# Performance work log

Hardware: AMD Instinct MI355X
Metric: run time of the kernel (lower is better)

The kernel has to match this reference:

```python
import jax, jax.numpy as jnp
import numpy as np

B, H, L, DK = 1, 16, 2048, 64
F_FACTOR = 64            # f
MAX_SEQ = 2048           # max_seq_len
RB = MAX_SEQ // F_FACTOR # 32, out dim of f_b


def setup_inputs() -> dict:
    key = jax.random.key(0)
    ks = jax.random.split(key, 6)
    q = jax.random.normal(ks[0], (B, H, L, DK), dtype=jnp.float32)
    v = jax.random.normal(ks[1], (B, H, L, DK), dtype=jnp.float32)
    # nn.Linear weights: [out_features, in_features]
    Wa = jax.random.normal(ks[2], (F_FACTOR, DK), dtype=jnp.float32) / np.sqrt(DK)
    ba = jax.random.normal(ks[3], (F_FACTOR,), dtype=jnp.float32) * 0.02
    Wb = jax.random.normal(ks[4], (RB, DK), dtype=jnp.float32) / np.sqrt(DK)
    bb = jax.random.normal(ks[5], (RB,), dtype=jnp.float32) * 0.02
    return {"q": q, "v": v, "Wa": Wa, "ba": ba, "Wb": Wb, "bb": bb, "len_q": L}


def reference(q, v, Wa, ba, Wb, bb, len_q):
    f = Wa.shape[0]            # f
    rb = Wb.shape[0]           # max_seq_len // f
    # h_a: repeat each of the f factor channels (max_seq_len//f) times -> [B,H,L,max_seq_len], slice to len_q
    h_a = jnp.repeat(q @ Wa.T + ba, rb, axis=-1)[..., :len_q]
    # h_b: repeat each of the (max_seq_len//f) channels f times
    h_b = jnp.repeat(q @ Wb.T + bb, f, axis=-1)[..., :len_q]
    # dense_attn = h_a @ h_b^T  -> [B,H,L,L]
    dense_attn = jnp.einsum('bhik,bhjk->bhij', h_a, h_b)
    # mask=None path; dropout inactive (eval / p=0)
    dense_attn = jax.nn.softmax(dense_attn, axis=-1)
    output = jnp.matmul(dense_attn, v)  # [B,H,L,DK]
    return (output, dense_attn)
```

## Files before the change

kernel.cpp:

```cpp
#include <hip/hip_runtime.h>
#include <hip/hip_bf16.h>


#define HN 16
#define LN 2048
#define KR 32

typedef __attribute__((ext_vector_type(8))) short bf16x8;
typedef __attribute__((ext_vector_type(4))) float f32x4;

__device__ __forceinline__ float b2f(unsigned short u) {
    return __uint_as_float(((unsigned int)u) << 16);
}
__device__ __forceinline__ unsigned short f2b(float f) {
    __hip_bfloat16 h = __float2bfloat16(f);
    return *reinterpret_cast<unsigned short*>(&h);
}
__device__ __forceinline__ void glds16(const void* g, void* l) {
    __builtin_amdgcn_global_load_lds(
        (const __attribute__((address_space(1))) unsigned int*)g,
        (__attribute__((address_space(3))) unsigned int*)l, 16, 0, 0);
}

#define TILE_SH 8192

__global__ __launch_bounds__(256) void k_cb(
    const float* __restrict__ q,
    const float* __restrict__ Wa, const float* __restrict__ ba,
    const float* __restrict__ Wb, const float* __restrict__ bb,
    unsigned short* __restrict__ Chi, unsigned short* __restrict__ Clo,
    unsigned short* __restrict__ Tile)
{
    __shared__ float sWa[64 * 64];
    __shared__ float sWb[32 * 64];
    __shared__ float sba[64];
    __shared__ float sbb[32];
    const int tid = threadIdx.x;
    for (int i = tid; i < 64 * 64; i += 256) sWa[i] = Wa[i];
    for (int i = tid; i < 32 * 64; i += 256) sWb[i] = Wb[i];
    if (tid < 64) sba[tid] = ba[tid];
    if (tid < 32) sbb[tid] = bb[tid];
    __syncthreads();

    const int t = blockIdx.x * 256 + tid;
    const int row = t >> 2, kg = t & 3, mh = kg * 8;
    const int h = row >> 11, i = row & 2047;
    const int jc = i >> 6, c = i & 63;

    float qf[64];
    const float4* q4p = reinterpret_cast<const float4*>(q + (size_t)row * 64);
    #pragma unroll
    for (int k4 = 0; k4 < 16; ++k4) {
        float4 u = q4p[k4];
        qf[4*k4+0] = u.x; qf[4*k4+1] = u.y; qf[4*k4+2] = u.z; qf[4*k4+3] = u.w;
    }
    unsigned short chb[8], clb[8], bhb[8], blb[8];
    #pragma unroll
    for (int mi = 0; mi < 8; ++mi) {
        const int m = mh + mi;
        float a0 = sba[2*m], a1 = sba[2*m+1], bv = sbb[m];
        const float4* wa0 = reinterpret_cast<const float4*>(&sWa[(2*m) * 64]);
        const float4* wa1 = reinterpret_cast<const float4*>(&sWa[(2*m+1) * 64]);
        const float4* wb0 = reinterpret_cast<const float4*>(&sWb[m * 64]);
        #pragma unroll
        for (int k4 = 0; k4 < 16; ++k4) {
            float4 w0 = wa0[k4], w1 = wa1[k4], w2 = wb0[k4];
            float x0 = qf[4*k4], x1 = qf[4*k4+1], x2 = qf[4*k4+2], x3 = qf[4*k4+3];
            a0 = fmaf(x0, w0.x, a0); a0 = fmaf(x1, w0.y, a0);
            a0 = fmaf(x2, w0.z, a0); a0 = fmaf(x3, w0.w, a0);
            a1 = fmaf(x0, w1.x, a1); a1 = fmaf(x1, w1.y, a1);
            a1 = fmaf(x2, w1.z, a1); a1 = fmaf(x3, w1.w, a1);
            bv = fmaf(x0, w2.x, bv); bv = fmaf(x1, w2.y, bv);
            bv = fmaf(x2, w2.z, bv); bv = fmaf(x3, w2.w, bv);
        }
        float cc = 32.f * (a0 + a1);
        unsigned short ch = f2b(cc);
        chb[mi] = ch; clb[mi] = f2b(cc - b2f(ch));
        unsigned short bh = f2b(bv);
        bhb[mi] = bh; blb[mi] = f2b(bv - b2f(bh));
    }
    *reinterpret_cast<uint4*>(Chi + (size_t)row * KR + mh) = *reinterpret_cast<uint4*>(chb);
    *reinterpret_cast<uint4*>(Clo + (size_t)row * KR + mh) = *reinterpret_cast<uint4*>(clb);
    unsigned short* tb = Tile + (size_t)(h * 32 + jc) * TILE_SH + (kg * 64 + c) * 8;
    *reinterpret_cast<uint4*>(tb)        = *reinterpret_cast<uint4*>(bhb);
    *reinterpret_cast<uint4*>(tb + 2048) = *reinterpret_cast<uint4*>(blb);
}

__global__ __launch_bounds__(256) void k_vtc(
    const float* __restrict__ v, unsigned short* __restrict__ Tile)
{
    __shared__ unsigned short sv[64 * 66];
    const int tid = threadIdx.x;
    const int h = blockIdx.x >> 5, jc = blockIdx.x & 31;
    const float* src = v + (size_t)(h * LN + jc * 64) * 64;
    for (int i = tid; i < 4096; i += 256)
        sv[(i >> 6) * 66 + (i & 63)] = f2b(src[i]);
    __syncthreads();
    unsigned short* vt = Tile + (size_t)(h * 32 + jc) * TILE_SH + 4096;
    #pragma unroll
    for (int it = 0; it < 2; ++it) {
        const int gi = tid + it * 256;
        const int jg = gi >> 6, d = gi & 63;
        unsigned short g8[8];
        #pragma unroll
        for (int cjj = 0; cjj < 8; ++cjj)
            g8[cjj] = sv[(jg * 8 + cjj) * 66 + d];
        *reinterpret_cast<uint4*>(vt + (jg * 64 + d) * 8) = *reinterpret_cast<uint4*>(g8);
    }
}

__global__ __launch_bounds__(256) void k_pvs(
    const unsigned short* __restrict__ Chi, const unsigned short* __restrict__ Clo,
    const unsigned short* __restrict__ Tile,
    float* __restrict__ outO, float* __restrict__ outP)
{
    __shared__ unsigned short sT[TILE_SH];
    __shared__ unsigned short Ps[4][16 * 68];
    __shared__ float Psf[4][16 * 68];
    const int b = blockIdx.x;
    const int h = (b & 7) * 2 + (b >> 8);
    const int tile = (b >> 3) & 31;
    const int tid = threadIdx.x, w = tid >> 6, lane = tid & 63;
    const int quad = lane >> 4, n16 = lane & 15;
    const int rbase = tile * 64 + w * 16;
    const int hL = h * LN;
    unsigned short* ps = &Ps[w][0];
    float* psf = &Psf[w][0];

    const bf16x8 ahi = *reinterpret_cast<const bf16x8*>(Chi + (size_t)(hL + rbase + n16) * KR + quad * 8);
    const bf16x8 alo = *reinterpret_cast<const bf16x8*>(Clo + (size_t)(hL + rbase + n16) * KR + quad * 8);

    const char* tBase = (const char*)(Tile + (size_t)(h * 32) * TILE_SH);
    char* sTb = (char*)sT;
    const int fragB = (quad * 64 + n16) * 8;
    const int lane16 = lane * 16;

    f32x4 zero = {0.f, 0.f, 0.f, 0.f};

    float m0[4] = {-1e30f, -1e30f, -1e30f, -1e30f};
    float l0[4] = {0.f, 0.f, 0.f, 0.f};
    for (int jc = 0; jc < 32; ++jc) {
        const char* g = tBase + (size_t)jc * (TILE_SH * 2);
        glds16(g + w * 1024 + lane16,      sTb + w * 1024);
        glds16(g + (w + 4) * 1024 + lane16, sTb + (w + 4) * 1024);
        __syncthreads();
        f32x4 s[4];
        #pragma unroll
        for (int ni = 0; ni < 4; ++ni) {
            bf16x8 bhi = *reinterpret_cast<const bf16x8*>(sT + fragB + ni * 128);
            bf16x8 blo = *reinterpret_cast<const bf16x8*>(sT + 2048 + fragB + ni * 128);
            f32x4 acc = zero;
            acc = __builtin_amdgcn_mfma_f32_16x16x32_bf16(ahi, bhi, acc, 0, 0, 0);
            acc = __builtin_amdgcn_mfma_f32_16x16x32_bf16(ahi, blo, acc, 0, 0, 0);
            acc = __builtin_amdgcn_mfma_f32_16x16x32_bf16(alo, bhi, acc, 0, 0, 0);
            acc = __builtin_amdgcn_mfma_f32_16x16x32_bf16(alo, blo, acc, 0, 0, 0);
            s[ni] = acc;
        }
        #pragma unroll
        for (int r = 0; r < 4; ++r) {
            float v0 = s[0][r], v1 = s[1][r], v2 = s[2][r], v3 = s[3][r];
            float mx = fmaxf(fmaxf(v0, v1), fmaxf(v2, v3));
            float mn = fmaxf(m0[r], mx);
            l0[r] = l0[r] * __expf(m0[r] - mn)
                  + __expf(v0 - mn) + __expf(v1 - mn)
                  + __expf(v2 - mn) + __expf(v3 - mn);
            m0[r] = mn;
        }
        __syncthreads();
    }
    #pragma unroll
    for (int off = 1; off <= 8; off <<= 1) {
        #pragma unroll
        for (int r = 0; r < 4; ++r) {
            float m2 = __shfl_xor(m0[r], off, 64);
            float l2 = __shfl_xor(l0[r], off, 64);
            float mn = fmaxf(m0[r], m2);
            l0[r] = l0[r] * __expf(m0[r] - mn) + l2 * __expf(m2 - mn);
            m0[r] = mn;
        }
    }
    float mr[4], li[4];
    #pragma unroll
    for (int r = 0; r < 4; ++r) { mr[r] = m0[r]; li[r] = 1.f / l0[r]; }

    f32x4 o[4];
    #pragma unroll
    for (int di = 0; di < 4; ++di) o[di] = zero;

    for (int jc = 0; jc < 32; ++jc) {
        const int jb = jc * 64;
        const char* g = tBase + (size_t)jc * (TILE_SH * 2);
        glds16(g + w * 1024 + lane16,        sTb + w * 1024);
        glds16(g + (w + 4) * 1024 + lane16,  sTb + (w + 4) * 1024);
        glds16(g + (w + 8) * 1024 + lane16,  sTb + (w + 8) * 1024);
        glds16(g + (w + 12) * 1024 + lane16, sTb + (w + 12) * 1024);
        __syncthreads();
        #pragma unroll
        for (int ni = 0; ni < 4; ++ni) {
            bf16x8 bhi = *reinterpret_cast<const bf16x8*>(sT + fragB + ni * 128);
            bf16x8 blo = *reinterpret_cast<const bf16x8*>(sT + 2048 + fragB + ni * 128);
            f32x4 acc = zero;
            acc = __builtin_amdgcn_mfma_f32_16x16x32_bf16(ahi, bhi, acc, 0, 0, 0);
            acc = __builtin_amdgcn_mfma_f32_16x16x32_bf16(ahi, blo, acc, 0, 0, 0);
            acc = __builtin_amdgcn_mfma_f32_16x16x32_bf16(alo, bhi, acc, 0, 0, 0);
            acc = __builtin_amdgcn_mfma_f32_16x16x32_bf16(alo, blo, acc, 0, 0, 0);
            #pragma unroll
            for (int r = 0; r < 4; ++r) {
                float p = __expf(acc[r] - mr[r]) * li[r];
                const int sidx = (quad * 4 + r) * 68 + ni * 16 + n16;
                psf[sidx] = p;
                ps[sidx] = f2b(p);
            }
        }
        #pragma unroll
        for (int rr = 0; rr < 4; ++rr) {
            const int prow = rr * 4 + quad;
            const int pcol = n16 * 4;
            f32x4 val = *reinterpret_cast<f32x4*>(psf + prow * 68 + pcol);
            __builtin_nontemporal_store(val,
                reinterpret_cast<f32x4*>(outP + (size_t)(hL + rbase + prow) * LN + jb + pcol));
        }
        #pragma unroll
        for (int ks = 0; ks < 2; ++ks) {
            const bf16x8 pa = *reinterpret_cast<const bf16x8*>(ps + n16 * 68 + ks * 32 + quad * 8);
            #pragma unroll
            for (int di = 0; di < 4; ++di) {
                const bf16x8 vb = *reinterpret_cast<const bf16x8*>(
                    sT + 4096 + ((ks * 4 + quad) * 64 + di * 16 + n16) * 8);
                o[di] = __builtin_amdgcn_mfma_f32_16x16x32_bf16(pa, vb, o[di], 0, 0, 0);
            }
        }
        __syncthreads();
    }
    #pragma unroll
    for (int di = 0; di < 4; ++di) {
        #pragma unroll
        for (int r = 0; r < 4; ++r) {
            const int grow = rbase + quad * 4 + r;
            __builtin_nontemporal_store(o[di][r],
                &outO[(size_t)(hL + grow) * 64 + di * 16 + n16]);
        }
    }
}

extern "C" void kernel_launch(void* const* d_in, const int* in_sizes, int n_in,
                              void* d_out, int out_size, void* d_ws, size_t ws_size,
                              hipStream_t stream)
{
    (void)in_sizes; (void)n_in; (void)out_size; (void)ws_size;
    const float* q  = (const float*)d_in[0];
    const float* v  = (const float*)d_in[1];
    const float* Wa = (const float*)d_in[2];
    const float* ba = (const float*)d_in[3];
    const float* Wb = (const float*)d_in[4];
    const float* bb = (const float*)d_in[5];

    float* out = (float*)d_out;
    char* wsb = (char*)d_ws;
    const size_t CBb = (size_t)HN * LN * KR * 2;
    unsigned short* Chi  = (unsigned short*)(wsb + 0 * CBb);
    unsigned short* Clo  = (unsigned short*)(wsb + 1 * CBb);
    unsigned short* Tile = (unsigned short*)(wsb + 2 * CBb);

    float* outO = out;
    float* outP = out + (size_t)HN * LN * 64;

    hipLaunchKernelGGL(k_cb, dim3(512), dim3(256), 0, stream,
                       q, Wa, ba, Wb, bb, Chi, Clo, Tile);
    hipLaunchKernelGGL(k_vtc, dim3(512), dim3(256), 0, stream, v, Tile);
    hipLaunchKernelGGL(k_pvs, dim3(512), dim3(256), 0, stream,
                       Chi, Clo, Tile, outO, outP);
}
```

Before: 389.4 us.

## Double-buffer LDS key/value tiles to prefetch next chunk during compute

The shared K/V tile buffer becomes two buffers. The next chunk's global-to-LDS async loads are issued right after the barrier, while the current chunk is computed, in both the stats pass and the output pass. This drops one barrier per iteration and hides global load latency behind the MFMA and exp work. In exchange, the tile buffer's LDS use doubles, which can lower how many blocks fit on each CU.

```diff
diff --git a/kernel.cpp b/kernel.cpp
--- a/kernel.cpp
+++ b/kernel.cpp
@@ -114,7 +114,7 @@
     const unsigned short* __restrict__ Tile,
     float* __restrict__ outO, float* __restrict__ outP)
 {
-    __shared__ unsigned short sT[TILE_SH];
+    __shared__ unsigned short sT[2][TILE_SH];
     __shared__ unsigned short Ps[4][16 * 68];
     __shared__ float Psf[4][16 * 68];
     const int b = blockIdx.x;
@@ -131,24 +131,33 @@
     const bf16x8 alo = *reinterpret_cast<const bf16x8*>(Clo + (size_t)(hL + rbase + n16) * KR + quad * 8);
 
     const char* tBase = (const char*)(Tile + (size_t)(h * 32) * TILE_SH);
-    char* sTb = (char*)sT;
     const int fragB = (quad * 64 + n16) * 8;
-    const int lane16 = lane * 16;
+    const int woff = w * 1024 + lane * 16;
 
     f32x4 zero = {0.f, 0.f, 0.f, 0.f};
 
     float m0[4] = {-1e30f, -1e30f, -1e30f, -1e30f};
     float l0[4] = {0.f, 0.f, 0.f, 0.f};
+    {
+        char* d = (char*)sT[0];
+        glds16(tBase + woff, d + w * 1024);
+        glds16(tBase + woff + 4096, d + w * 1024 + 4096);
+    }
     for (int jc = 0; jc < 32; ++jc) {
-        const char* g = tBase + (size_t)jc * (TILE_SH * 2);
-        glds16(g + w * 1024 + lane16,      sTb + w * 1024);
-        glds16(g + (w + 4) * 1024 + lane16, sTb + (w + 4) * 1024);
         __syncthreads();
+        const int cur = jc & 1;
+        if (jc + 1 < 32) {
+            const char* g = tBase + (size_t)(jc + 1) * (TILE_SH * 2);
+            char* d = (char*)sT[cur ^ 1];
+            glds16(g + woff, d + w * 1024);
+            glds16(g + woff + 4096, d + w * 1024 + 4096);
+        }
+        const unsigned short* t = sT[cur];
         f32x4 s[4];
         #pragma unroll
         for (int ni = 0; ni < 4; ++ni) {
-            bf16x8 bhi = *reinterpret_cast<const bf16x8*>(sT + fragB + ni * 128);
-            bf16x8 blo = *reinterpret_cast<const bf16x8*>(sT + 2048 + fragB + ni * 128);
+            bf16x8 bhi = *reinterpret_cast<const bf16x8*>(t + fragB + ni * 128);
+            bf16x8 blo = *reinterpret_cast<const bf16x8*>(t + 2048 + fragB + ni * 128);
             f32x4 acc = zero;
             acc = __builtin_amdgcn_mfma_f32_16x16x32_bf16(ahi, bhi, acc, 0, 0, 0);
             acc = __builtin_amdgcn_mfma_f32_16x16x32_bf16(ahi, blo, acc, 0, 0, 0);
@@ -166,7 +175,13 @@
                   + __expf(v2 - mn) + __expf(v3 - mn);
             m0[r] = mn;
         }
-        __syncthreads();
+    }
+    {
+        char* d = (char*)sT[0];
+        glds16(tBase + woff, d + w * 1024);
+        glds16(tBase + woff + 4096, d + w * 1024 + 4096);
+        glds16(tBase + woff + 8192, d + w * 1024 + 8192);
+        glds16(tBase + woff + 12288, d + w * 1024 + 12288);
     }
     #pragma unroll
     for (int off = 1; off <= 8; off <<= 1) {
@@ -188,17 +203,22 @@
     for (int di = 0; di < 4; ++di) o[di] = zero;
 
     for (int jc = 0; jc < 32; ++jc) {
+        __syncthreads();
+        const int cur = jc & 1;
+        if (jc + 1 < 32) {
+            const char* g = tBase + (size_t)(jc + 1) * (TILE_SH * 2);
+            char* d = (char*)sT[cur ^ 1];
+            glds16(g + woff, d + w * 1024);
+            glds16(g + woff + 4096, d + w * 1024 + 4096);
+            glds16(g + woff + 8192, d + w * 1024 + 8192);
+            glds16(g + woff + 12288, d + w * 1024 + 12288);
+        }
+        const unsigned short* t = sT[cur];
         const int jb = jc * 64;
-        const char* g = tBase + (size_t)jc * (TILE_SH * 2);
-        glds16(g + w * 1024 + lane16,        sTb + w * 1024);
-        glds16(g + (w + 4) * 1024 + lane16,  sTb + (w + 4) * 1024);
-        glds16(g + (w + 8) * 1024 + lane16,  sTb + (w + 8) * 1024);
-        glds16(g + (w + 12) * 1024 + lane16, sTb + (w + 12) * 1024);
-        __syncthreads();
         #pragma unroll
         for (int ni = 0; ni < 4; ++ni) {
-            bf16x8 bhi = *reinterpret_cast<const bf16x8*>(sT + fragB + ni * 128);
-            bf16x8 blo = *reinterpret_cast<const bf16x8*>(sT + 2048 + fragB + ni * 128);
+            bf16x8 bhi = *reinterpret_cast<const bf16x8*>(t + fragB + ni * 128);
+            bf16x8 blo = *reinterpret_cast<const bf16x8*>(t + 2048 + fragB + ni * 128);
             f32x4 acc = zero;
             acc = __builtin_amdgcn_mfma_f32_16x16x32_bf16(ahi, bhi, acc, 0, 0, 0);
             acc = __builtin_amdgcn_mfma_f32_16x16x32_bf16(ahi, blo, acc, 0, 0, 0);
@@ -226,11 +246,10 @@
             #pragma unroll
             for (int di = 0; di < 4; ++di) {
                 const bf16x8 vb = *reinterpret_cast<const bf16x8*>(
-                    sT + 4096 + ((ks * 4 + quad) * 64 + di * 16 + n16) * 8);
+                    t + 4096 + ((ks * 4 + quad) * 64 + di * 16 + n16) * 8);
                 o[di] = __builtin_amdgcn_mfma_f32_16x16x32_bf16(pa, vb, o[di], 0, 0, 0);
             }
         }
-        __syncthreads();
     }
     #pragma unroll
     for (int di = 0; di < 4; ++di) {
```

After: 389.3 us. Within noise of the previous version (-0.0%).

## Compute each row block's scores once in registers and double-buffer B/V tiles

Applied to the files above, without the earlier changes.

The fused kernel now handles 16 query rows per block (2048 blocks), with the four waves splitting each 64-column chunk. It computes all scores once and keeps them in registers, doing an exact max/sum softmax with a cross-wave LDS reduction, so the second QK recompute pass is gone. The B and V tiles are split into separate buffers and double-buffered with async global-to-LDS loads, and the P·V product is accumulated per wave then normalized at the end. The lo×lo correction MFMA is dropped. Holding 32 score vectors per thread raises register pressure, the P stores are now scalar, and precision drops slightly.

```diff
diff --git a/kernel.cpp b/kernel.cpp
--- a/kernel.cpp
+++ b/kernel.cpp
@@ -22,14 +22,15 @@
         (__attribute__((address_space(3))) unsigned int*)l, 16, 0, 0);
 }
 
-#define TILE_SH 8192
+#define TILE_B 4096
+#define TILE_V 4096
 
 __global__ __launch_bounds__(256) void k_cb(
     const float* __restrict__ q,
     const float* __restrict__ Wa, const float* __restrict__ ba,
     const float* __restrict__ Wb, const float* __restrict__ bb,
     unsigned short* __restrict__ Chi, unsigned short* __restrict__ Clo,
-    unsigned short* __restrict__ Tile)
+    unsigned short* __restrict__ TileB)
 {
     __shared__ float sWa[64 * 64];
     __shared__ float sWb[32 * 64];
@@ -81,13 +82,13 @@
     }
     *reinterpret_cast<uint4*>(Chi + (size_t)row * KR + mh) = *reinterpret_cast<uint4*>(chb);
     *reinterpret_cast<uint4*>(Clo + (size_t)row * KR + mh) = *reinterpret_cast<uint4*>(clb);
-    unsigned short* tb = Tile + (size_t)(h * 32 + jc) * TILE_SH + (kg * 64 + c) * 8;
+    unsigned short* tb = TileB + (size_t)(h * 32 + jc) * TILE_B + (kg * 64 + c) * 8;
     *reinterpret_cast<uint4*>(tb)        = *reinterpret_cast<uint4*>(bhb);
     *reinterpret_cast<uint4*>(tb + 2048) = *reinterpret_cast<uint4*>(blb);
 }
 
 __global__ __launch_bounds__(256) void k_vtc(
-    const float* __restrict__ v, unsigned short* __restrict__ Tile)
+    const float* __restrict__ v, unsigned short* __restrict__ TileV)
 {
     __shared__ unsigned short sv[64 * 66];
     const int tid = threadIdx.x;
@@ -96,151 +97,165 @@
     for (int i = tid; i < 4096; i += 256)
         sv[(i >> 6) * 66 + (i & 63)] = f2b(src[i]);
     __syncthreads();
-    unsigned short* vt = Tile + (size_t)(h * 32 + jc) * TILE_SH + 4096;
+    unsigned short* vt = TileV + (size_t)(h * 32 + jc) * TILE_V;
     #pragma unroll
     for (int it = 0; it < 2; ++it) {
         const int gi = tid + it * 256;
         const int jg = gi >> 6, d = gi & 63;
         unsigned short g8[8];
         #pragma unroll
-        for (int cjj = 0; cjj < 8; ++cjj)
-            g8[cjj] = sv[(jg * 8 + cjj) * 66 + d];
+        for (int jj = 0; jj < 8; ++jj)
+            g8[jj] = sv[(jg * 8 + jj) * 66 + d];
         *reinterpret_cast<uint4*>(vt + (jg * 64 + d) * 8) = *reinterpret_cast<uint4*>(g8);
     }
 }
 
-__global__ __launch_bounds__(256) void k_pvs(
+__global__ __launch_bounds__(256, 2) void k_fuse(
     const unsigned short* __restrict__ Chi, const unsigned short* __restrict__ Clo,
-    const unsigned short* __restrict__ Tile,
+    const unsigned short* __restrict__ TileB, const unsigned short* __restrict__ TileV,
     float* __restrict__ outO, float* __restrict__ outP)
 {
-    __shared__ unsigned short sT[TILE_SH];
-    __shared__ unsigned short Ps[4][16 * 68];
-    __shared__ float Psf[4][16 * 68];
+    __shared__ unsigned short sB[2][TILE_B];
+    __shared__ unsigned short sV[2][TILE_V];
+    __shared__ unsigned short ps[2][16 * 72];
+    __shared__ float sRedM[4][16];
+    __shared__ float sRedL[4][16];
+
     const int b = blockIdx.x;
-    const int h = (b & 7) * 2 + (b >> 8);
-    const int tile = (b >> 3) & 31;
+    const int h = (b & 7) * 2 + (b >> 10);
+    const int tile = (b >> 3) & 127;
     const int tid = threadIdx.x, w = tid >> 6, lane = tid & 63;
     const int quad = lane >> 4, n16 = lane & 15;
-    const int rbase = tile * 64 + w * 16;
+    const int rbase = tile * 16;
     const int hL = h * LN;
-    unsigned short* ps = &Ps[w][0];
-    float* psf = &Psf[w][0];
 
     const bf16x8 ahi = *reinterpret_cast<const bf16x8*>(Chi + (size_t)(hL + rbase + n16) * KR + quad * 8);
     const bf16x8 alo = *reinterpret_cast<const bf16x8*>(Clo + (size_t)(hL + rbase + n16) * KR + quad * 8);
 
-    const char* tBase = (const char*)(Tile + (size_t)(h * 32) * TILE_SH);
-    char* sTb = (char*)sT;
-    const int fragB = (quad * 64 + n16) * 8;
-    const int lane16 = lane * 16;
+    const char* bBase = (const char*)(TileB + (size_t)(h * 32) * TILE_B);
+    const char* vBase = (const char*)(TileV + (size_t)(h * 32) * TILE_V);
+    const int srcOff = w * 2048 + lane * 16;
+    const int fragW = (quad * 64 + w * 16 + n16) * 8;
 
     f32x4 zero = {0.f, 0.f, 0.f, 0.f};
-
-    float m0[4] = {-1e30f, -1e30f, -1e30f, -1e30f};
-    float l0[4] = {0.f, 0.f, 0.f, 0.f};
+    f32x4 sS[32];
+
+    {
+        char* d = (char*)sB[0];
+        glds16(bBase + srcOff,        d + w * 2048);
+        glds16(bBase + srcOff + 1024, d + w * 2048 + 1024);
+    }
+    #pragma unroll
     for (int jc = 0; jc < 32; ++jc) {
-        const char* g = tBase + (size_t)jc * (TILE_SH * 2);
-        glds16(g + w * 1024 + lane16,      sTb + w * 1024);
-        glds16(g + (w + 4) * 1024 + lane16, sTb + (w + 4) * 1024);
-        __syncthreads();
-        f32x4 s[4];
-        #pragma unroll
-        for (int ni = 0; ni < 4; ++ni) {
-            bf16x8 bhi = *reinterpret_cast<const bf16x8*>(sT + fragB + ni * 128);
-            bf16x8 blo = *reinterpret_cast<const bf16x8*>(sT + 2048 + fragB + ni * 128);
-            f32x4 acc = zero;
-            acc = __builtin_amdgcn_mfma_f32_16x16x32_bf16(ahi, bhi, acc, 0, 0, 0);
-            acc = __builtin_amdgcn_mfma_f32_16x16x32_bf16(ahi, blo, acc, 0, 0, 0);
-            acc = __builtin_amdgcn_mfma_f32_16x16x32_bf16(alo, bhi, acc, 0, 0, 0);
-            acc = __builtin_amdgcn_mfma_f32_16x16x32_bf16(alo, blo, acc, 0, 0, 0);
-            s[ni] = acc;
-        }
+        const int cur = jc & 1;
+        __syncthreads();
+        if (jc + 1 < 32) {
+            const char* g = bBase + (size_t)(jc + 1) * (TILE_B * 2);
+            char* d = (char*)sB[cur ^ 1];
+            glds16(g + srcOff,        d + w * 2048);
+            glds16(g + srcOff + 1024, d + w * 2048 + 1024);
+        }
+        const unsigned short* t = sB[cur];
+        bf16x8 bhi = *reinterpret_cast<const bf16x8*>(t + fragW);
+        bf16x8 blo = *reinterpret_cast<const bf16x8*>(t + 2048 + fragW);
+        f32x4 acc = zero;
+        acc = __builtin_amdgcn_mfma_f32_16x16x32_bf16(ahi, bhi, acc, 0, 0, 0);
+        acc = __builtin_amdgcn_mfma_f32_16x16x32_bf16(ahi, blo, acc, 0, 0, 0);
+        acc = __builtin_amdgcn_mfma_f32_16x16x32_bf16(alo, bhi, acc, 0, 0, 0);
+        sS[jc] = acc;
+    }
+
+    float mr[4], li[4];
+    {
+        float m0[4];
         #pragma unroll
         for (int r = 0; r < 4; ++r) {
-            float v0 = s[0][r], v1 = s[1][r], v2 = s[2][r], v3 = s[3][r];
-            float mx = fmaxf(fmaxf(v0, v1), fmaxf(v2, v3));
-            float mn = fmaxf(m0[r], mx);
-            l0[r] = l0[r] * __expf(m0[r] - mn)
-                  + __expf(v0 - mn) + __expf(v1 - mn)
-                  + __expf(v2 - mn) + __expf(v3 - mn);
-            m0[r] = mn;
-        }
-        __syncthreads();
-    }
-    #pragma unroll
-    for (int off = 1; off <= 8; off <<= 1) {
+            float mm = sS[0][r];
+            #pragma unroll
+            for (int jc = 1; jc < 32; ++jc) mm = fmaxf(mm, sS[jc][r]);
+            #pragma unroll
+            for (int off = 1; off <= 8; off <<= 1)
+                mm = fmaxf(mm, __shfl_xor(mm, off, 64));
+            m0[r] = mm;
+        }
+        __syncthreads();
+        if (n16 == 0) {
+            #pragma unroll
+            for (int r = 0; r < 4; ++r) sRedM[w][quad * 4 + r] = m0[r];
+        }
+        __syncthreads();
+        #pragma unroll
+        for (int r = 0; r < 4; ++r)
+            mr[r] = fmaxf(fmaxf(sRedM[0][quad*4+r], sRedM[1][quad*4+r]),
+                          fmaxf(sRedM[2][quad*4+r], sRedM[3][quad*4+r]));
+        float l0[4] = {0.f, 0.f, 0.f, 0.f};
+        #pragma unroll
+        for (int jc = 0; jc < 32; ++jc) {
+            #pragma unroll
+            for (int r = 0; r < 4; ++r) {
+                float p = __expf(sS[jc][r] - mr[r]);
+                sS[jc][r] = p;
+                l0[r] += p;
+            }
+        }
         #pragma unroll
         for (int r = 0; r < 4; ++r) {
-            float m2 = __shfl_xor(m0[r], off, 64);
-            float l2 = __shfl_xor(l0[r], off, 64);
-            float mn = fmaxf(m0[r], m2);
-            l0[r] = l0[r] * __expf(m0[r] - mn) + l2 * __expf(m2 - mn);
-            m0[r] = mn;
-        }
-    }
-    float mr[4], li[4];
-    #pragma unroll
-    for (int r = 0; r < 4; ++r) { mr[r] = m0[r]; li[r] = 1.f / l0[r]; }
-
-    f32x4 o[4];
-    #pragma unroll
-    for (int di = 0; di < 4; ++di) o[di] = zero;
-
+            float ll = l0[r];
+            #pragma unroll
+            for (int off = 1; off <= 8; off <<= 1)
+                ll += __shfl_xor(ll, off, 64);
+            l0[r] = ll;
+        }
+        if (n16 == 0) {
+            #pragma unroll
+            for (int r = 0; r < 4; ++r) sRedL[w][quad * 4 + r] = l0[r];
+        }
+        __syncthreads();
+        #pragma unroll
+        for (int r = 0; r < 4; ++r)
+            li[r] = 1.f / (sRedL[0][quad*4+r] + sRedL[1][quad*4+r]
+                         + sRedL[2][quad*4+r] + sRedL[3][quad*4+r]);
+    }
+
+    f32x4 o = zero;
+    {
+        char* d = (char*)sV[0];
+        glds16(vBase + srcOff,        d + w * 2048);
+        glds16(vBase + srcOff + 1024, d + w * 2048 + 1024);
+        #pragma unroll
+        for (int r = 0; r < 4; ++r)
+            ps[0][(quad * 4 + r) * 72 + w * 16 + n16] = f2b(sS[0][r]);
+    }
+    #pragma unroll
     for (int jc = 0; jc < 32; ++jc) {
+        const int cur = jc & 1;
+        __syncthreads();
+        if (jc + 1 < 32) {
+            const char* g = vBase + (size_t)(jc + 1) * (TILE_V * 2);
+            char* d = (char*)sV[cur ^ 1];
+            glds16(g + srcOff,        d + w * 2048);
+            glds16(g + srcOff + 1024, d + w * 2048 + 1024);
+            #pragma unroll
+            for (int r = 0; r < 4; ++r)
+                ps[cur ^ 1][(quad * 4 + r) * 72 + w * 16 + n16] = f2b(sS[jc + 1][r]);
+        }
         const int jb = jc * 64;
-        const char* g = tBase + (size_t)jc * (TILE_SH * 2);
-        glds16(g + w * 1024 + lane16,        sTb + w * 1024);
-        glds16(g + (w + 4) * 1024 + lane16,  sTb + (w + 4) * 1024);
-        glds16(g + (w + 8) * 1024 + lane16,  sTb + (w + 8) * 1024);
-        glds16(g + (w + 12) * 1024 + lane16, sTb + (w + 12) * 1024);
-        __syncthreads();
-        #pragma unroll
-        for (int ni = 0; ni < 4; ++ni) {
-            bf16x8 bhi = *reinterpret_cast<const bf16x8*>(sT + fragB + ni * 128);
-            bf16x8 blo = *reinterpret_cast<const bf16x8*>(sT + 2048 + fragB + ni * 128);
-            f32x4 acc = zero;
-            acc = __builtin_amdgcn_mfma_f32_16x16x32_bf16(ahi, bhi, acc, 0, 0, 0);
-            acc = __builtin_amdgcn_mfma_f32_16x16x32_bf16(ahi, blo, acc, 0, 0, 0);
-            acc = __builtin_amdgcn_mfma_f32_16x16x32_bf16(alo, bhi, acc, 0, 0, 0);
-            acc = __builtin_amdgcn_mfma_f32_16x16x32_bf16(alo, blo, acc, 0, 0, 0);
-            #pragma unroll
-            for (int r = 0; r < 4; ++r) {
-                float p = __expf(acc[r] - mr[r]) * li[r];
-                const int sidx = (quad * 4 + r) * 68 + ni * 16 + n16;
-                psf[sidx] = p;
-                ps[sidx] = f2b(p);
-            }
-        }
-        #pragma unroll
-        for (int rr = 0; rr < 4; ++rr) {
-            const int prow = rr * 4 + quad;
-            const int pcol = n16 * 4;
-            f32x4 val = *reinterpret_cast<f32x4*>(psf + prow * 68 + pcol);
-            __builtin_nontemporal_store(val,
-                reinterpret_cast<f32x4*>(outP + (size_t)(hL + rbase + prow) * LN + jb + pcol));
-        }
+        #pragma unroll
+        for (int r = 0; r < 4; ++r)
+            __builtin_nontemporal_store(sS[jc][r] * li[r],
+                outP + (size_t)(hL + rbase + quad * 4 + r) * LN + jb + w * 16 + n16);
         #pragma unroll
         for (int ks = 0; ks < 2; ++ks) {
-            const bf16x8 pa = *reinterpret_cast<const bf16x8*>(ps + n16 * 68 + ks * 32 + quad * 8);
-            #pragma unroll
-            for (int di = 0; di < 4; ++di) {
-                const bf16x8 vb = *reinterpret_cast<const bf16x8*>(
-                    sT + 4096 + ((ks * 4 + quad) * 64 + di * 16 + n16) * 8);
-                o[di] = __builtin_amdgcn_mfma_f32_16x16x32_bf16(pa, vb, o[di], 0, 0, 0);
-            }
-        }
-        __syncthreads();
-    }
-    #pragma unroll
-    for (int di = 0; di < 4; ++di) {
-        #pragma unroll
-        for (int r = 0; r < 4; ++r) {
-            const int grow = rbase + quad * 4 + r;
-            __builtin_nontemporal_store(o[di][r],
-                &outO[(size_t)(hL + grow) * 64 + di * 16 + n16]);
-        }
-    }
+            bf16x8 pa = *reinterpret_cast<const bf16x8*>(&ps[cur][n16 * 72 + ks * 32 + quad * 8]);
+            bf16x8 vb = *reinterpret_cast<const bf16x8*>(
+                sV[cur] + ((ks * 4 + quad) * 64 + w * 16 + n16) * 8);
+            o = __builtin_amdgcn_mfma_f32_16x16x32_bf16(pa, vb, o, 0, 0, 0);
+        }
+    }
+    #pragma unroll
+    for (int r = 0; r < 4; ++r)
+        __builtin_nontemporal_store(o[r] * li[r],
+            &outO[(size_t)(hL + rbase + quad * 4 + r) * 64 + w * 16 + n16]);
 }
 
 extern "C" void kernel_launch(void* const* d_in, const int* in_sizes, int n_in,
@@ -257,17 +272,18 @@
 
     float* out = (float*)d_out;
     char* wsb = (char*)d_ws;
-    const size_t CBb = (size_t)HN * LN * KR * 2;
-    unsigned short* Chi  = (unsigned short*)(wsb + 0 * CBb);
-    unsigned short* Clo  = (unsigned short*)(wsb + 1 * CBb);
-    unsigned short* Tile = (unsigned short*)(wsb + 2 * CBb);
+    const size_t MB = 1024 * 1024;
+    unsigned short* Chi   = (unsigned short*)(wsb);
+    unsigned short* Clo   = (unsigned short*)(wsb + 2 * MB);
+    unsigned short* TileB = (unsigned short*)(wsb + 4 * MB);
+    unsigned short* TileV = (unsigned short*)(wsb + 8 * MB);
 
     float* outO = out;
     float* outP = out + (size_t)HN * LN * 64;
 
     hipLaunchKernelGGL(k_cb, dim3(512), dim3(256), 0, stream,
-                       q, Wa, ba, Wb, bb, Chi, Clo, Tile);
-    hipLaunchKernelGGL(k_vtc, dim3(512), dim3(256), 0, stream, v, Tile);
-    hipLaunchKernelGGL(k_pvs, dim3(512), dim3(256), 0, stream,
-                       Chi, Clo, Tile, outO, outP);
-}
+                       q, Wa, ba, Wb, bb, Chi, Clo, TileB);
+    hipLaunchKernelGGL(k_vtc, dim3(512), dim3(256), 0, stream, v, TileV);
+    hipLaunchKernelGGL(k_fuse, dim3(2048), dim3(256), 0, stream,
+                       Chi, Clo, TileB, TileV, outO, outP);
+}
```

Result: slower. 412.0 us (+5.8%).
